# Optimization experiments

Measured on AMD Instinct MI355X. Metric: run time of the kernel, lower is better.

The kernel has to match this reference:

```python
import jax, jax.numpy as jnp
import numpy as np

TWO_PI = 2.0 * np.pi


def setup_inputs() -> dict:
    key = jax.random.key(0)
    k1, k2 = jax.random.split(key)
    B, N, F = 1, 4096, 4096
    query_points = jax.random.normal(k1, (B, N, 3), dtype=jnp.float32)
    face_coord = jax.random.normal(k2, (B, F, 3, 3), dtype=jnp.float32)
    return {"query_points": query_points, "face_coord": face_coord}


def _winding(query_points, face_coord):
    # query_points: [B, N, 3]; face_coord: [B, F, 3, 3]
    # Per-pair vectors from query point to each triangle vertex: [B, N, F, 3]
    qp = query_points[:, :, None, :]  # [B, N, 1, 3]
    a = face_coord[:, None, :, 0, :] - qp
    b = face_coord[:, None, :, 1, :] - qp
    c = face_coord[:, None, :, 2, :] - qp

    det = jnp.sum(a * jnp.cross(b, c), axis=-1)          # [B, N, F]
    na = jnp.linalg.norm(a, axis=-1)
    nb = jnp.linalg.norm(b, axis=-1)
    nc = jnp.linalg.norm(c, axis=-1)
    ab = jnp.sum(a * b, axis=-1)
    bc = jnp.sum(b * c, axis=-1)
    ac = jnp.sum(a * c, axis=-1)

    denom = na * nb * nc + bc * na + ac * nb + ab * nc
    solid_angle_2 = jnp.arctan2(det, denom)              # [B, N, F]
    # Sum solid angles over all faces, normalize by 2*pi -> winding number/occupancy
    return jnp.sum(solid_angle_2, axis=-1) / TWO_PI      # [B, N]


def reference(query_points, face_coord):
    return _winding(query_points, face_coord)
```

## Files before the change

### kernel.cpp

```cpp
#include <hip/hip_runtime.h>
#include <math.h>

#define N_Q 4096
#define N_F 4096
#define QPT 2
#define QBLK (256 * QPT)
#define FSPLIT 128
#define FT (N_F / FSPLIT)
#define INV_2PI 0.15915494309189535f

__device__ __forceinline__ float fast_atan2f(float y, float x) {
    const float pi   = 3.14159265358979f;
    const float pi_2 = 1.57079632679490f;
    float ax = fabsf(x), ay = fabsf(y);
    float mx = fmaxf(ax, ay), mn = fminf(ax, ay);
    mx = fmaxf(mx, 1e-30f);
    float t = mn * __builtin_amdgcn_rcpf(mx);
    float s = t * t;
    float p =              -0.0117212f;
    p = fmaf(p, s,  0.05265332f);
    p = fmaf(p, s, -0.11643287f);
    p = fmaf(p, s,  0.19354346f);
    p = fmaf(p, s, -0.33262347f);
    p = fmaf(p, s,  0.99997726f);
    float r = p * t;
    r = (ay > ax) ? (pi_2 - r) : r;
    r = (x < 0.0f) ? (pi - r) : r;
    return copysignf(r, y);
}

__device__ __forceinline__ float pair_term(
    float qx, float qy, float qz, float th,
    float4 A, float4 B, float4 C, float4 Nv, float4 K)
{
    const float da  = fmaf(-qx, A.x, fmaf(-qy, A.y, fmaf(-qz, A.z, th)));
    const float db  = fmaf(-qx, B.x, fmaf(-qy, B.y, fmaf(-qz, B.z, th)));
    const float dc  = fmaf(-qx, C.x, fmaf(-qy, C.y, fmaf(-qz, C.z, th)));
    const float det = fmaf(-qx, Nv.x, fmaf(-qy, Nv.y, fmaf(-qz, Nv.z, Nv.w)));

    const float na = __builtin_amdgcn_sqrtf(fmaf(2.0f, da, A.w));
    const float nb = __builtin_amdgcn_sqrtf(fmaf(2.0f, db, B.w));
    const float nc = __builtin_amdgcn_sqrtf(fmaf(2.0f, dc, C.w));

    const float ab = K.x + (da + db);
    const float bc = K.y + (db + dc);
    const float ac = K.z + (da + dc);

    const float denom = fmaf(na * nb, nc, fmaf(bc, na, fmaf(ac, nb, ab * nc)));
    return fast_atan2f(det, denom);
}

__global__ __launch_bounds__(256) void winding_kernel(
    const float* __restrict__ qp,
    const float* __restrict__ fc,
    float* __restrict__ out)
{
    __shared__ float  raw[FT * 9];
    __shared__ float4 cst[FT][5];

    const int tid = threadIdx.x;

    for (int i = tid; i < FT * 9; i += 256)
        raw[i] = fc[(size_t)blockIdx.y * FT * 9 + i];
    __syncthreads();

    if (tid < FT) {
        const float* v = &raw[tid * 9];
        const float ax = v[0], ay = v[1], az = v[2];
        const float bx = v[3], by = v[4], bz = v[5];
        const float cx = v[6], cy = v[7], cz = v[8];
        const float ux = by*cz - bz*cy, uy = bz*cx - bx*cz, uz = bx*cy - by*cx;
        const float vx = cy*az - cz*ay, vy = cz*ax - cx*az, vz = cx*ay - cy*ax;
        const float wx = ay*bz - az*by, wy = az*bx - ax*bz, wz = ax*by - ay*bx;
        const float D  = ax*ux + ay*uy + az*uz;
        cst[tid][0] = make_float4(ax, ay, az, ax*ax + ay*ay + az*az);
        cst[tid][1] = make_float4(bx, by, bz, bx*bx + by*by + bz*bz);
        cst[tid][2] = make_float4(cx, cy, cz, cx*cx + cy*cy + cz*cz);
        cst[tid][3] = make_float4(ux + vx + wx, uy + vy + wy, uz + vz + wz, D);
        cst[tid][4] = make_float4(ax*bx + ay*by + az*bz,
                                  bx*cx + by*cy + bz*cz,
                                  ax*cx + ay*cy + az*cz, 0.0f);
    }
    __syncthreads();

    const int q0 = blockIdx.x * QBLK + tid;
    const int q1 = q0 + 256;
    const float q0x = qp[q0*3+0], q0y = qp[q0*3+1], q0z = qp[q0*3+2];
    const float q1x = qp[q1*3+0], q1y = qp[q1*3+1], q1z = qp[q1*3+2];
    const float th0 = 0.5f * fmaf(q0x, q0x, fmaf(q0y, q0y, q0z * q0z));
    const float th1 = 0.5f * fmaf(q1x, q1x, fmaf(q1y, q1y, q1z * q1z));

    float s0 = 0.0f, s1 = 0.0f;
    #pragma unroll 4
    for (int f = 0; f < FT; ++f) {
        const float4 A  = cst[f][0];
        const float4 B  = cst[f][1];
        const float4 C  = cst[f][2];
        const float4 Nv = cst[f][3];
        const float4 K  = cst[f][4];
        s0 += pair_term(q0x, q0y, q0z, th0, A, B, C, Nv, K);
        s1 += pair_term(q1x, q1y, q1z, th1, A, B, C, Nv, K);
    }

    atomicAdd(&out[q0], s0 * INV_2PI);
    atomicAdd(&out[q1], s1 * INV_2PI);
}

extern "C" void kernel_launch(void* const* d_in, const int* in_sizes, int n_in,
                              void* d_out, int out_size, void* d_ws, size_t ws_size,
                              hipStream_t stream) {
    const float* qp = (const float*)d_in[0];
    const float* fc = (const float*)d_in[1];
    float* out = (float*)d_out;

    hipMemsetAsync(out, 0, (size_t)out_size * sizeof(float), stream);

    dim3 grid(N_Q / QBLK, FSPLIT);
    dim3 block(256);
    winding_kernel<<<grid, block, 0, stream>>>(qp, fc, out);
}
```

Measured before the change: 28.64 us.

## Precompute face constants in separate kernel and use packed f32x2 FMA math

Moves the per-face constant computation into its own kernel that writes to workspace. The main kernel then reads those constants straight from global memory (uniform, scalar-cacheable loads), with no LDS staging and no barriers. It also packs the two query points per thread into f32x2 vectors so the FMAs can map to packed FP32 instructions, and lowers the unroll factor. The cost is an extra kernel launch, plus reliance on the workspace size, with an LDS fallback path when it is too small.

```diff
diff --git a/kernel.cpp b/kernel.cpp
--- a/kernel.cpp
+++ b/kernel.cpp
@@ -8,6 +8,13 @@
 #define FSPLIT 128
 #define FT (N_F / FSPLIT)
 #define INV_2PI 0.15915494309189535f
+
+typedef __attribute__((ext_vector_type(2))) float f32x2;
+
+static __device__ __forceinline__ f32x2 fma2(f32x2 a, f32x2 b, f32x2 c) {
+    return __builtin_elementwise_fma(a, b, c);
+}
+static __device__ __forceinline__ f32x2 splat(float x) { return (f32x2){x, x}; }
 
 __device__ __forceinline__ float fast_atan2f(float y, float x) {
     const float pi   = 3.14159265358979f;
@@ -29,41 +36,83 @@
     return copysignf(r, y);
 }
 
-__device__ __forceinline__ float pair_term(
-    float qx, float qy, float qz, float th,
-    float4 A, float4 B, float4 C, float4 Nv, float4 K)
+__global__ __launch_bounds__(256) void face_const_kernel(
+    const float* __restrict__ fc, float4* __restrict__ cst)
 {
-    const float da  = fmaf(-qx, A.x, fmaf(-qy, A.y, fmaf(-qz, A.z, th)));
-    const float db  = fmaf(-qx, B.x, fmaf(-qy, B.y, fmaf(-qz, B.z, th)));
-    const float dc  = fmaf(-qx, C.x, fmaf(-qy, C.y, fmaf(-qz, C.z, th)));
-    const float det = fmaf(-qx, Nv.x, fmaf(-qy, Nv.y, fmaf(-qz, Nv.z, Nv.w)));
-
-    const float na = __builtin_amdgcn_sqrtf(fmaf(2.0f, da, A.w));
-    const float nb = __builtin_amdgcn_sqrtf(fmaf(2.0f, db, B.w));
-    const float nc = __builtin_amdgcn_sqrtf(fmaf(2.0f, dc, C.w));
-
-    const float ab = K.x + (da + db);
-    const float bc = K.y + (db + dc);
-    const float ac = K.z + (da + dc);
-
-    const float denom = fmaf(na * nb, nc, fmaf(bc, na, fmaf(ac, nb, ab * nc)));
-    return fast_atan2f(det, denom);
+    const int f = blockIdx.x * 256 + threadIdx.x;
+    if (f >= N_F) return;
+    const float* v = fc + (size_t)f * 9;
+    const float ax = v[0], ay = v[1], az = v[2];
+    const float bx = v[3], by = v[4], bz = v[5];
+    const float cx = v[6], cy = v[7], cz = v[8];
+    const float ux = by*cz - bz*cy, uy = bz*cx - bx*cz, uz = bx*cy - by*cx;
+    const float vx = cy*az - cz*ay, vy = cz*ax - cx*az, vz = cx*ay - cy*ax;
+    const float wx = ay*bz - az*by, wy = az*bx - ax*bz, wz = ax*by - ay*bx;
+    const float D  = ax*ux + ay*uy + az*uz;
+    float4* o = cst + (size_t)f * 5;
+    o[0] = make_float4(ax, ay, az, ax*ax + ay*ay + az*az);
+    o[1] = make_float4(bx, by, bz, bx*bx + by*by + bz*bz);
+    o[2] = make_float4(cx, cy, cz, cx*cx + cy*cy + cz*cz);
+    o[3] = make_float4(ux + vx + wx, uy + vy + wy, uz + vz + wz, D);
+    o[4] = make_float4(ax*bx + ay*by + az*bz,
+                       bx*cx + by*cy + bz*cz,
+                       ax*cx + ay*cy + az*cz, 0.0f);
 }
 
-__global__ __launch_bounds__(256) void winding_kernel(
-    const float* __restrict__ qp,
-    const float* __restrict__ fc,
+__global__ __launch_bounds__(256) void winding_packed(
+    const float* __restrict__ qp, const float4* __restrict__ cst,
+    float* __restrict__ out)
+{
+    const int tid = threadIdx.x;
+    const int q0 = blockIdx.x * QBLK + tid;
+    const int q1 = q0 + 256;
+    const int f0 = blockIdx.y * FT;
+
+    const f32x2 qx = {qp[q0*3+0], qp[q1*3+0]};
+    const f32x2 qy = {qp[q0*3+1], qp[q1*3+1]};
+    const f32x2 qz = {qp[q0*3+2], qp[q1*3+2]};
+    const f32x2 th = 0.5f * fma2(qx, qx, fma2(qy, qy, qz * qz));
+
+    f32x2 s = {0.0f, 0.0f};
+    #pragma unroll 2
+    for (int f = 0; f < FT; ++f) {
+        const float4* cf = cst + (size_t)(f0 + f) * 5;
+        const float4 A = cf[0], B = cf[1], C = cf[2], Nv = cf[3], K = cf[4];
+
+        const f32x2 da  = fma2(-qx, splat(A.x), fma2(-qy, splat(A.y), fma2(-qz, splat(A.z), th)));
+        const f32x2 db  = fma2(-qx, splat(B.x), fma2(-qy, splat(B.y), fma2(-qz, splat(B.z), th)));
+        const f32x2 dc  = fma2(-qx, splat(C.x), fma2(-qy, splat(C.y), fma2(-qz, splat(C.z), th)));
+        const f32x2 det = fma2(-qx, splat(Nv.x), fma2(-qy, splat(Nv.y), fma2(-qz, splat(Nv.z), splat(Nv.w))));
+
+        const f32x2 ra = fma2(splat(2.0f), da, splat(A.w));
+        const f32x2 rb = fma2(splat(2.0f), db, splat(B.w));
+        const f32x2 rc = fma2(splat(2.0f), dc, splat(C.w));
+        const f32x2 na = { __builtin_amdgcn_sqrtf(ra.x), __builtin_amdgcn_sqrtf(ra.y) };
+        const f32x2 nb = { __builtin_amdgcn_sqrtf(rb.x), __builtin_amdgcn_sqrtf(rb.y) };
+        const f32x2 nc = { __builtin_amdgcn_sqrtf(rc.x), __builtin_amdgcn_sqrtf(rc.y) };
+
+        const f32x2 ab = splat(K.x) + (da + db);
+        const f32x2 bc = splat(K.y) + (db + dc);
+        const f32x2 ac = splat(K.z) + (da + dc);
+
+        const f32x2 den = fma2(na * nb, nc, fma2(bc, na, fma2(ac, nb, ab * nc)));
+        s += (f32x2){ fast_atan2f(det.x, den.x), fast_atan2f(det.y, den.y) };
+    }
+
+    atomicAdd(&out[q0], s.x * INV_2PI);
+    atomicAdd(&out[q1], s.y * INV_2PI);
+}
+
+__global__ __launch_bounds__(256) void winding_lds(
+    const float* __restrict__ qp, const float* __restrict__ fc,
     float* __restrict__ out)
 {
     __shared__ float  raw[FT * 9];
-    __shared__ float4 cst[FT][5];
-
+    __shared__ float4 cstl[FT][5];
     const int tid = threadIdx.x;
-
     for (int i = tid; i < FT * 9; i += 256)
         raw[i] = fc[(size_t)blockIdx.y * FT * 9 + i];
     __syncthreads();
-
     if (tid < FT) {
         const float* v = &raw[tid * 9];
         const float ax = v[0], ay = v[1], az = v[2];
@@ -73,37 +122,45 @@
         const float vx = cy*az - cz*ay, vy = cz*ax - cx*az, vz = cx*ay - cy*ax;
         const float wx = ay*bz - az*by, wy = az*bx - ax*bz, wz = ax*by - ay*bx;
         const float D  = ax*ux + ay*uy + az*uz;
-        cst[tid][0] = make_float4(ax, ay, az, ax*ax + ay*ay + az*az);
-        cst[tid][1] = make_float4(bx, by, bz, bx*bx + by*by + bz*bz);
-        cst[tid][2] = make_float4(cx, cy, cz, cx*cx + cy*cy + cz*cz);
-        cst[tid][3] = make_float4(ux + vx + wx, uy + vy + wy, uz + vz + wz, D);
-        cst[tid][4] = make_float4(ax*bx + ay*by + az*bz,
-                                  bx*cx + by*cy + bz*cz,
-                                  ax*cx + ay*cy + az*cz, 0.0f);
+        cstl[tid][0] = make_float4(ax, ay, az, ax*ax + ay*ay + az*az);
+        cstl[tid][1] = make_float4(bx, by, bz, bx*bx + by*by + bz*bz);
+        cstl[tid][2] = make_float4(cx, cy, cz, cx*cx + cy*cy + cz*cz);
+        cstl[tid][3] = make_float4(ux + vx + wx, uy + vy + wy, uz + vz + wz, D);
+        cstl[tid][4] = make_float4(ax*bx + ay*by + az*bz, bx*cx + by*cy + bz*cz,
+                                   ax*cx + ay*cy + az*cz, 0.0f);
     }
     __syncthreads();
 
     const int q0 = blockIdx.x * QBLK + tid;
     const int q1 = q0 + 256;
-    const float q0x = qp[q0*3+0], q0y = qp[q0*3+1], q0z = qp[q0*3+2];
-    const float q1x = qp[q1*3+0], q1y = qp[q1*3+1], q1z = qp[q1*3+2];
-    const float th0 = 0.5f * fmaf(q0x, q0x, fmaf(q0y, q0y, q0z * q0z));
-    const float th1 = 0.5f * fmaf(q1x, q1x, fmaf(q1y, q1y, q1z * q1z));
+    const f32x2 qx = {qp[q0*3+0], qp[q1*3+0]};
+    const f32x2 qy = {qp[q0*3+1], qp[q1*3+1]};
+    const f32x2 qz = {qp[q0*3+2], qp[q1*3+2]};
+    const f32x2 th = 0.5f * fma2(qx, qx, fma2(qy, qy, qz * qz));
 
-    float s0 = 0.0f, s1 = 0.0f;
-    #pragma unroll 4
+    f32x2 s = {0.0f, 0.0f};
+    #pragma unroll 2
     for (int f = 0; f < FT; ++f) {
-        const float4 A  = cst[f][0];
-        const float4 B  = cst[f][1];
-        const float4 C  = cst[f][2];
-        const float4 Nv = cst[f][3];
-        const float4 K  = cst[f][4];
-        s0 += pair_term(q0x, q0y, q0z, th0, A, B, C, Nv, K);
-        s1 += pair_term(q1x, q1y, q1z, th1, A, B, C, Nv, K);
+        const float4 A = cstl[f][0], B = cstl[f][1], C = cstl[f][2];
+        const float4 Nv = cstl[f][3], K = cstl[f][4];
+        const f32x2 da  = fma2(-qx, splat(A.x), fma2(-qy, splat(A.y), fma2(-qz, splat(A.z), th)));
+        const f32x2 db  = fma2(-qx, splat(B.x), fma2(-qy, splat(B.y), fma2(-qz, splat(B.z), th)));
+        const f32x2 dc  = fma2(-qx, splat(C.x), fma2(-qy, splat(C.y), fma2(-qz, splat(C.z), th)));
+        const f32x2 det = fma2(-qx, splat(Nv.x), fma2(-qy, splat(Nv.y), fma2(-qz, splat(Nv.z), splat(Nv.w))));
+        const f32x2 ra = fma2(splat(2.0f), da, splat(A.w));
+        const f32x2 rb = fma2(splat(2.0f), db, splat(B.w));
+        const f32x2 rc = fma2(splat(2.0f), dc, splat(C.w));
+        const f32x2 na = { __builtin_amdgcn_sqrtf(ra.x), __builtin_amdgcn_sqrtf(ra.y) };
+        const f32x2 nb = { __builtin_amdgcn_sqrtf(rb.x), __builtin_amdgcn_sqrtf(rb.y) };
+        const f32x2 nc = { __builtin_amdgcn_sqrtf(rc.x), __builtin_amdgcn_sqrtf(rc.y) };
+        const f32x2 ab = splat(K.x) + (da + db);
+        const f32x2 bc = splat(K.y) + (db + dc);
+        const f32x2 ac = splat(K.z) + (da + dc);
+        const f32x2 den = fma2(na * nb, nc, fma2(bc, na, fma2(ac, nb, ab * nc)));
+        s += (f32x2){ fast_atan2f(det.x, den.x), fast_atan2f(det.y, den.y) };
     }
-
-    atomicAdd(&out[q0], s0 * INV_2PI);
-    atomicAdd(&out[q1], s1 * INV_2PI);
+    atomicAdd(&out[q0], s.x * INV_2PI);
+    atomicAdd(&out[q1], s.y * INV_2PI);
 }
 
 extern "C" void kernel_launch(void* const* d_in, const int* in_sizes, int n_in,
@@ -115,7 +172,15 @@
 
     hipMemsetAsync(out, 0, (size_t)out_size * sizeof(float), stream);
 
+    const size_t ws_needed = (size_t)N_F * 5 * sizeof(float4);
     dim3 grid(N_Q / QBLK, FSPLIT);
     dim3 block(256);
-    winding_kernel<<<grid, block, 0, stream>>>(qp, fc, out);
+
+    if (ws_size >= ws_needed) {
+        float4* cst = (float4*)d_ws;
+        face_const_kernel<<<dim3(N_F / 256), block, 0, stream>>>(fc, cst);
+        winding_packed<<<grid, block, 0, stream>>>(qp, cst, out);
+    } else {
+        winding_lds<<<grid, block, 0, stream>>>(qp, fc, out);
+    }
 }
```

Result: slower. 32.73 us (+14.3%).

## Combine four atan2 terms via complex multiplication before a single atan2

Applied to the files above, without the earlier changes.

Replaces per-face atan2 with complex-number products that merge the angles of four faces, tracking 2π wraparounds in a separate correction counter, so only one atan2 is evaluated per four faces. It also vectorises the face load into shared memory with float4 copies. The aim is to cut transcendental/ALU work in the inner loop. The price is extra multiplies, sign logic, and risk of overflow or precision loss when products of large magnitudes are chained. The wrap detection may also be wrong in edge cases.

```diff
diff --git a/kernel.cpp b/kernel.cpp
--- a/kernel.cpp
+++ b/kernel.cpp
@@ -29,14 +29,25 @@
     return copysignf(r, y);
 }
 
-__device__ __forceinline__ float pair_term(
+__device__ __forceinline__ void merge_angle(
+    float y1, float x1, float y2, float x2,
+    float& ym, float& xm, float& w)
+{
+    ym = fmaf(y1, x2, y2 * x1);
+    xm = fmaf(-y1, y2, x1 * x2);
+    const float c = copysignf(1.0f, y1) + copysignf(1.0f, y2);
+    w += (ym * c < 0.0f) ? 0.5f * c : 0.0f;
+}
+
+__device__ __forceinline__ void build_dn(
     float qx, float qy, float qz, float th,
-    float4 A, float4 B, float4 C, float4 Nv, float4 K)
+    float4 A, float4 B, float4 C, float4 Nv, float4 K,
+    float& det, float& den)
 {
-    const float da  = fmaf(-qx, A.x, fmaf(-qy, A.y, fmaf(-qz, A.z, th)));
-    const float db  = fmaf(-qx, B.x, fmaf(-qy, B.y, fmaf(-qz, B.z, th)));
-    const float dc  = fmaf(-qx, C.x, fmaf(-qy, C.y, fmaf(-qz, C.z, th)));
-    const float det = fmaf(-qx, Nv.x, fmaf(-qy, Nv.y, fmaf(-qz, Nv.z, Nv.w)));
+    const float da = fmaf(-qx, A.x, fmaf(-qy, A.y, fmaf(-qz, A.z, th)));
+    const float db = fmaf(-qx, B.x, fmaf(-qy, B.y, fmaf(-qz, B.z, th)));
+    const float dc = fmaf(-qx, C.x, fmaf(-qy, C.y, fmaf(-qz, C.z, th)));
+    det = fmaf(-qx, Nv.x, fmaf(-qy, Nv.y, fmaf(-qz, Nv.z, Nv.w)));
 
     const float na = __builtin_amdgcn_sqrtf(fmaf(2.0f, da, A.w));
     const float nb = __builtin_amdgcn_sqrtf(fmaf(2.0f, db, B.w));
@@ -46,8 +57,7 @@
     const float bc = K.y + (db + dc);
     const float ac = K.z + (da + dc);
 
-    const float denom = fmaf(na * nb, nc, fmaf(bc, na, fmaf(ac, nb, ab * nc)));
-    return fast_atan2f(det, denom);
+    den = fmaf(na * nb, nc, fmaf(bc, na, fmaf(ac, nb, ab * nc)));
 }
 
 __global__ __launch_bounds__(256) void winding_kernel(
@@ -60,8 +70,11 @@
 
     const int tid = threadIdx.x;
 
-    for (int i = tid; i < FT * 9; i += 256)
-        raw[i] = fc[(size_t)blockIdx.y * FT * 9 + i];
+    {
+        const float4* src = (const float4*)(fc + (size_t)blockIdx.y * FT * 9);
+        float4* dst = (float4*)raw;
+        if (tid < FT * 9 / 4) dst[tid] = src[tid];
+    }
     __syncthreads();
 
     if (tid < FT) {
@@ -90,20 +103,43 @@
     const float th0 = 0.5f * fmaf(q0x, q0x, fmaf(q0y, q0y, q0z * q0z));
     const float th1 = 0.5f * fmaf(q1x, q1x, fmaf(q1y, q1y, q1z * q1z));
 
-    float s0 = 0.0f, s1 = 0.0f;
-    #pragma unroll 4
-    for (int f = 0; f < FT; ++f) {
-        const float4 A  = cst[f][0];
-        const float4 B  = cst[f][1];
-        const float4 C  = cst[f][2];
-        const float4 Nv = cst[f][3];
-        const float4 K  = cst[f][4];
-        s0 += pair_term(q0x, q0y, q0z, th0, A, B, C, Nv, K);
-        s1 += pair_term(q1x, q1y, q1z, th1, A, B, C, Nv, K);
+    float s0 = 0.0f, w0 = 0.0f;
+    float s1 = 0.0f, w1 = 0.0f;
+
+    for (int f = 0; f < FT; f += 4) {
+        const float4 A0 = cst[f+0][0], B0 = cst[f+0][1], C0 = cst[f+0][2], N0 = cst[f+0][3], K0 = cst[f+0][4];
+        const float4 A1 = cst[f+1][0], B1 = cst[f+1][1], C1 = cst[f+1][2], N1 = cst[f+1][3], K1 = cst[f+1][4];
+        const float4 A2 = cst[f+2][0], B2 = cst[f+2][1], C2 = cst[f+2][2], N2 = cst[f+2][3], K2 = cst[f+2][4];
+        const float4 A3 = cst[f+3][0], B3 = cst[f+3][1], C3 = cst[f+3][2], N3 = cst[f+3][3], K3 = cst[f+3][4];
+
+        {
+            float d0,n0,d1,n1,d2,n2,d3,n3;
+            build_dn(q0x,q0y,q0z,th0, A0,B0,C0,N0,K0, d0,n0);
+            build_dn(q0x,q0y,q0z,th0, A1,B1,C1,N1,K1, d1,n1);
+            build_dn(q0x,q0y,q0z,th0, A2,B2,C2,N2,K2, d2,n2);
+            build_dn(q0x,q0y,q0z,th0, A3,B3,C3,N3,K3, d3,n3);
+            float ya,xa,yb,xb,Y,X;
+            merge_angle(d0,n0, d1,n1, ya,xa, w0);
+            merge_angle(d2,n2, d3,n3, yb,xb, w0);
+            merge_angle(ya,xa, yb,xb, Y, X,  w0);
+            s0 += fast_atan2f(Y, X);
+        }
+        {
+            float d0,n0,d1,n1,d2,n2,d3,n3;
+            build_dn(q1x,q1y,q1z,th1, A0,B0,C0,N0,K0, d0,n0);
+            build_dn(q1x,q1y,q1z,th1, A1,B1,C1,N1,K1, d1,n1);
+            build_dn(q1x,q1y,q1z,th1, A2,B2,C2,N2,K2, d2,n2);
+            build_dn(q1x,q1y,q1z,th1, A3,B3,C3,N3,K3, d3,n3);
+            float ya,xa,yb,xb,Y,X;
+            merge_angle(d0,n0, d1,n1, ya,xa, w1);
+            merge_angle(d2,n2, d3,n3, yb,xb, w1);
+            merge_angle(ya,xa, yb,xb, Y, X,  w1);
+            s1 += fast_atan2f(Y, X);
+        }
     }
 
-    atomicAdd(&out[q0], s0 * INV_2PI);
-    atomicAdd(&out[q1], s1 * INV_2PI);
+    atomicAdd(&out[q0], fmaf(s0, INV_2PI, w0));
+    atomicAdd(&out[q1], fmaf(s1, INV_2PI, w1));
 }
 
 extern "C" void kernel_launch(void* const* d_in, const int* in_sizes, int n_in,
```

New measurement: 29.10 us. About the same (+1.6%).
